# Kernel tuning notes

Measured on AMD Instinct MI355X. Metric: run time of the kernel, lower is better.

Reference implementation:

```python
import jax, jax.numpy as jnp
import numpy as np

IN_DIM, HID_DIM, OUT_DIM = 256, 1024, 256
B, T = 256, 512

def setup_inputs() -> dict:
    key = jax.random.key(0)
    ks = jax.random.split(key, 7)
    s_x = 1.0 / np.sqrt(IN_DIM)
    s_h = 1.0 / np.sqrt(HID_DIM)
    return {
        "x": jax.random.normal(ks[0], (B, T, IN_DIM), dtype=jnp.float32),
        "Wx": jax.random.uniform(ks[1], (3 * HID_DIM, IN_DIM), jnp.float32, -s_x, s_x),
        "bx": jax.random.uniform(ks[2], (3 * HID_DIM,), jnp.float32, -s_x, s_x),
        "Wh": jax.random.uniform(ks[3], (3 * HID_DIM, HID_DIM), jnp.float32, -s_h, s_h),
        "bh": jax.random.uniform(ks[4], (3 * HID_DIM,), jnp.float32, -s_h, s_h),
        "Wf": jax.random.uniform(ks[5], (OUT_DIM, HID_DIM), jnp.float32, -s_h, s_h),
        "bf": jax.random.uniform(ks[6], (OUT_DIM,), jnp.float32, -s_h, s_h),
    }

def _gru(x, Wx, bx, Wh, bh):
    # Precompute input projections for all timesteps: [B,T,3H]
    x_proj = jnp.einsum('bti,gi->btg', x, Wx) + bx
    h0 = jnp.zeros((x.shape[0], Wh.shape[1]), dtype=x.dtype)

    def step(h_prev, xp_t):
        h_t = h_prev @ Wh.T + bh  # [B,3H]
        x_r, x_z, x_n = jnp.split(xp_t, 3, axis=1)
        h_r, h_z, h_n = jnp.split(h_t, 3, axis=1)
        r = jax.nn.sigmoid(x_r + h_r)
        z = jax.nn.sigmoid(x_z + h_z)
        n = jnp.tanh(x_n + r * h_n)
        h = (1.0 - z) * h_prev + z * n  # note: nonstandard (follows source)
        return h, None

    h_final, _ = jax.lax.scan(step, h0, jnp.swapaxes(x_proj, 0, 1))
    return h_final

def reference(x, Wx, bx, Wh, bh, Wf, bf):
    h = _gru(x, Wx, bx, Wh, bh)
    return h @ Wf.T + bf  # [B, out_dim]
```

## Files before the change

### kernel.cpp

```cpp
#include <hip/hip_runtime.h>
#include <math.h>
#include <stddef.h>

#define BB 256
#define TT 512
#define IND 256
#define HH 1024
#define OUTD 256

#define INNER(ACC2)                                                            \
  _Pragma("unroll 8")                                                          \
  for (int c = 0; c < 32; ++c) {                                               \
    const float4 a  = *reinterpret_cast<const float4*>(&As[c][tb4]);           \
    const float4 w0 = *reinterpret_cast<const float4*>(&Ws[0][c][tj4]);        \
    const float4 w1 = *reinterpret_cast<const float4*>(&Ws[1][c][tj4]);        \
    const float4 w2 = *reinterpret_cast<const float4*>(&Ws[2][c][tj4]);        \
    const float av[4]  = {a.x, a.y, a.z, a.w};                                 \
    const float w0v[4] = {w0.x, w0.y, w0.z, w0.w};                             \
    const float w1v[4] = {w1.x, w1.y, w1.z, w1.w};                             \
    const float w2v[4] = {w2.x, w2.y, w2.z, w2.w};                             \
    _Pragma("unroll") for (int i = 0; i < 4; ++i) {                            \
      _Pragma("unroll") for (int l = 0; l < 4; ++l) {                          \
        acc[0][i][l] += av[i] * w0v[l];                                        \
        acc[1][i][l] += av[i] * w1v[l];                                        \
        ACC2[i][l]   += av[i] * w2v[l];                                        \
      }                                                                        \
    }                                                                          \
  }

__global__ __launch_bounds__(256) void step_gemm(
    const float* __restrict__ x, const float* __restrict__ Wx,
    const float* __restrict__ Wh, const float* __restrict__ h_prev,
    float* __restrict__ P, float* __restrict__ Pnh, int t)
{
  __shared__ float As[32][68];
  __shared__ float Ws[3][32][68];
  const int tid = threadIdx.x;
  const int b0 = blockIdx.x * 64;
  const int j0 = blockIdx.y * 64;
  const int z  = blockIdx.z;
  const int kg0 = z * 320;

  float acc[3][4][4] = {};
  float accnh[4][4]  = {};

  const int tj4 = (tid & 15) * 4;
  const int tb4 = (tid >> 4) * 4;

  const int a_row = tid >> 3;
  const int a_c4  = (tid & 7) * 4;

  for (int s = 0; s < 10; ++s) {
    const int kg = kg0 + s * 32;
    const bool isx = (kg < 256);
    __syncthreads();
    #pragma unroll
    for (int rr = 0; rr < 64; rr += 32) {
      const int b = b0 + a_row + rr;
      float4 v;
      if (isx) v = *reinterpret_cast<const float4*>(
                     &x[((size_t)b * TT + t) * IND + kg + a_c4]);
      else     v = *reinterpret_cast<const float4*>(
                     &h_prev[(size_t)b * HH + (kg - 256) + a_c4]);
      As[a_c4 + 0][a_row + rr] = v.x;
      As[a_c4 + 1][a_row + rr] = v.y;
      As[a_c4 + 2][a_row + rr] = v.z;
      As[a_c4 + 3][a_row + rr] = v.w;
    }
    #pragma unroll
    for (int p = 0; p < 6; ++p) {
      const int f   = tid + 256 * p;
      const int row = f >> 3;
      const int c4  = (f & 7) * 4;
      const int g   = row >> 6;
      const int jj  = row & 63;
      const int j   = j0 + jj;
      float4 v;
      if (isx) v = *reinterpret_cast<const float4*>(
                     &Wx[((size_t)g * HH + j) * IND + kg + c4]);
      else     v = *reinterpret_cast<const float4*>(
                     &Wh[((size_t)g * HH + j) * HH + (kg - 256) + c4]);
      Ws[g][c4 + 0][jj] = v.x;
      Ws[g][c4 + 1][jj] = v.y;
      Ws[g][c4 + 2][jj] = v.z;
      Ws[g][c4 + 3][jj] = v.w;
    }
    __syncthreads();

    const bool use_nh = (!isx) && (z == 0);
    if (use_nh) { INNER(accnh) } else { INNER(acc[2]) }
  }

  const size_t plane = (size_t)BB * HH;
  const int jout = j0 + tj4;
  #pragma unroll
  for (int g = 0; g < 3; ++g) {
    #pragma unroll
    for (int i = 0; i < 4; ++i) {
      const int b = b0 + tb4 + i;
      float4 v = {acc[g][i][0], acc[g][i][1], acc[g][i][2], acc[g][i][3]};
      *reinterpret_cast<float4*>(
        &P[((size_t)(z * 3 + g)) * plane + (size_t)b * HH + jout]) = v;
    }
  }
  if (z == 0) {
    #pragma unroll
    for (int i = 0; i < 4; ++i) {
      const int b = b0 + tb4 + i;
      float4 v = {accnh[i][0], accnh[i][1], accnh[i][2], accnh[i][3]};
      *reinterpret_cast<float4*>(&Pnh[(size_t)b * HH + jout]) = v;
    }
  }
}

__global__ __launch_bounds__(256) void gate_kernel(
    const float* __restrict__ P, const float* __restrict__ Pnh,
    const float* __restrict__ bx, const float* __restrict__ bh,
    const float* __restrict__ h_prev, float* __restrict__ h_next)
{
  const int cell = blockIdx.x * 256 + threadIdx.x;
  const int j = cell & (HH - 1);
  const size_t bj = (size_t)cell;
  const size_t plane = (size_t)BB * HH;

  float sr = bx[j] + bh[j];
  float sz = bx[HH + j] + bh[HH + j];
  #pragma unroll
  for (int k = 0; k < 4; ++k) {
    sr += P[((size_t)(k * 3 + 0)) * plane + bj];
    sz += P[((size_t)(k * 3 + 1)) * plane + bj];
  }
  float xn = P[2 * plane + bj] + bx[2 * HH + j];
  float hn = Pnh[bj] + bh[2 * HH + j];
  #pragma unroll
  for (int k = 1; k < 4; ++k) hn += P[((size_t)(k * 3 + 2)) * plane + bj];

  const float r  = 1.f / (1.f + __expf(-sr));
  const float zz = 1.f / (1.f + __expf(-sz));
  const float n  = tanhf(xn + r * hn);
  const float hp = h_prev[bj];
  h_next[bj] = (1.f - zz) * hp + zz * n;
}

__global__ __launch_bounds__(256) void final_gemm(
    const float* __restrict__ h, const float* __restrict__ Wf,
    const float* __restrict__ bf, float* __restrict__ out)
{
  __shared__ float As[32][36];
  __shared__ float Ws[32][36];
  const int tid = threadIdx.x;
  const int b0 = blockIdx.x * 32, o0 = blockIdx.y * 32;
  const int to = tid & 31, tb = tid >> 5;
  float acc[4] = {};
  for (int kc = 0; kc < HH; kc += 32) {
    __syncthreads();
    #pragma unroll
    for (int p = 0; p < 4; ++p) {
      const int f = tid + 256 * p;
      const int row = f >> 5, c = f & 31;
      As[c][row] = h[(size_t)(b0 + row) * HH + kc + c];
      Ws[c][row] = Wf[(size_t)(o0 + row) * HH + kc + c];
    }
    __syncthreads();
    #pragma unroll
    for (int c = 0; c < 32; ++c) {
      const float4 a = *reinterpret_cast<const float4*>(&As[c][tb * 4]);
      const float w = Ws[c][to];
      acc[0] += a.x * w; acc[1] += a.y * w; acc[2] += a.z * w; acc[3] += a.w * w;
    }
  }
  #pragma unroll
  for (int i = 0; i < 4; ++i)
    out[(size_t)(b0 + tb * 4 + i) * OUTD + o0 + to] = acc[i] + bf[o0 + to];
}

__global__ void zero_h(float* __restrict__ h)
{
  const int i = blockIdx.x * 256 + threadIdx.x;
  reinterpret_cast<float4*>(h)[i] = float4{0.f, 0.f, 0.f, 0.f};
}

extern "C" void kernel_launch(void* const* d_in, const int* in_sizes, int n_in,
                              void* d_out, int out_size, void* d_ws, size_t ws_size,
                              hipStream_t stream)
{
  const float* x  = (const float*)d_in[0];
  const float* Wx = (const float*)d_in[1];
  const float* bx = (const float*)d_in[2];
  const float* Wh = (const float*)d_in[3];
  const float* bh = (const float*)d_in[4];
  const float* Wf = (const float*)d_in[5];
  const float* bf = (const float*)d_in[6];
  float* out = (float*)d_out;

  float* ws = (float*)d_ws;
  const size_t plane = (size_t)BB * HH;
  float* h0  = ws;
  float* h1  = ws + plane;
  float* P   = ws + 2 * plane;
  float* Pnh = ws + 14 * plane;

  zero_h<<<256, 256, 0, stream>>>(h0);

  float* cur = h0;
  float* nxt = h1;
  for (int t = 0; t < TT; ++t) {
    step_gemm<<<dim3(4, 16, 4), 256, 0, stream>>>(x, Wx, Wh, cur, P, Pnh, t);
    gate_kernel<<<dim3(1024), 256, 0, stream>>>(P, Pnh, bx, bh, cur, nxt);
    float* tmp = cur; cur = nxt; nxt = tmp;
  }
  final_gemm<<<dim3(8, 8), 256, 0, stream>>>(cur, Wf, bf, out);
}
```

Measured before the change: 23.91 ms.

## Use split-bf16 MFMA GEMM with fused gates in a single per-step kernel

Result: slower. 30.09 ms (+25.9%).

```diff
diff --git a/kernel.cpp b/kernel.cpp
--- a/kernel.cpp
+++ b/kernel.cpp
@@ -8,138 +8,162 @@
 #define HH 1024
 #define OUTD 256
 
-#define INNER(ACC2)                                                            \
-  _Pragma("unroll 8")                                                          \
-  for (int c = 0; c < 32; ++c) {                                               \
-    const float4 a  = *reinterpret_cast<const float4*>(&As[c][tb4]);           \
-    const float4 w0 = *reinterpret_cast<const float4*>(&Ws[0][c][tj4]);        \
-    const float4 w1 = *reinterpret_cast<const float4*>(&Ws[1][c][tj4]);        \
-    const float4 w2 = *reinterpret_cast<const float4*>(&Ws[2][c][tj4]);        \
-    const float av[4]  = {a.x, a.y, a.z, a.w};                                 \
-    const float w0v[4] = {w0.x, w0.y, w0.z, w0.w};                             \
-    const float w1v[4] = {w1.x, w1.y, w1.z, w1.w};                             \
-    const float w2v[4] = {w2.x, w2.y, w2.z, w2.w};                             \
-    _Pragma("unroll") for (int i = 0; i < 4; ++i) {                            \
-      _Pragma("unroll") for (int l = 0; l < 4; ++l) {                          \
-        acc[0][i][l] += av[i] * w0v[l];                                        \
-        acc[1][i][l] += av[i] * w1v[l];                                        \
-        ACC2[i][l]   += av[i] * w2v[l];                                        \
-      }                                                                        \
-    }                                                                          \
-  }
-
-__global__ __launch_bounds__(256) void step_gemm(
-    const float* __restrict__ x, const float* __restrict__ Wx,
-    const float* __restrict__ Wh, const float* __restrict__ h_prev,
-    float* __restrict__ P, float* __restrict__ Pnh, int t)
-{
-  __shared__ float As[32][68];
-  __shared__ float Ws[3][32][68];
-  const int tid = threadIdx.x;
-  const int b0 = blockIdx.x * 64;
-  const int j0 = blockIdx.y * 64;
-  const int z  = blockIdx.z;
-  const int kg0 = z * 320;
-
-  float acc[3][4][4] = {};
-  float accnh[4][4]  = {};
-
-  const int tj4 = (tid & 15) * 4;
-  const int tb4 = (tid >> 4) * 4;
-
-  const int a_row = tid >> 3;
-  const int a_c4  = (tid & 7) * 4;
-
-  for (int s = 0; s < 10; ++s) {
-    const int kg = kg0 + s * 32;
-    const bool isx = (kg < 256);
-    __syncthreads();
-    #pragma unroll
-    for (int rr = 0; rr < 64; rr += 32) {
-      const int b = b0 + a_row + rr;
-      float4 v;
-      if (isx) v = *reinterpret_cast<const float4*>(
-                     &x[((size_t)b * TT + t) * IND + kg + a_c4]);
-      else     v = *reinterpret_cast<const float4*>(
-                     &h_prev[(size_t)b * HH + (kg - 256) + a_c4]);
-      As[a_c4 + 0][a_row + rr] = v.x;
-      As[a_c4 + 1][a_row + rr] = v.y;
-      As[a_c4 + 2][a_row + rr] = v.z;
-      As[a_c4 + 3][a_row + rr] = v.w;
-    }
-    #pragma unroll
-    for (int p = 0; p < 6; ++p) {
-      const int f   = tid + 256 * p;
-      const int row = f >> 3;
-      const int c4  = (f & 7) * 4;
-      const int g   = row >> 6;
-      const int jj  = row & 63;
-      const int j   = j0 + jj;
-      float4 v;
-      if (isx) v = *reinterpret_cast<const float4*>(
-                     &Wx[((size_t)g * HH + j) * IND + kg + c4]);
-      else     v = *reinterpret_cast<const float4*>(
-                     &Wh[((size_t)g * HH + j) * HH + (kg - 256) + c4]);
-      Ws[g][c4 + 0][jj] = v.x;
-      Ws[g][c4 + 1][jj] = v.y;
-      Ws[g][c4 + 2][jj] = v.z;
-      Ws[g][c4 + 3][jj] = v.w;
-    }
-    __syncthreads();
-
-    const bool use_nh = (!isx) && (z == 0);
-    if (use_nh) { INNER(accnh) } else { INNER(acc[2]) }
-  }
-
-  const size_t plane = (size_t)BB * HH;
-  const int jout = j0 + tj4;
+typedef __attribute__((ext_vector_type(8))) short short8;
+typedef __attribute__((ext_vector_type(4))) float f32x4;
+
+#define MFMA __builtin_amdgcn_mfma_f32_16x16x32_bf16
+
+__device__ __forceinline__ unsigned short bf16_rne(float f) {
+  unsigned u = __builtin_bit_cast(unsigned, f);
+  u += 0x7FFFu + ((u >> 16) & 1u);
+  return (unsigned short)(u >> 16);
+}
+__device__ __forceinline__ float bf16_f(unsigned short h) {
+  unsigned u = ((unsigned)h) << 16;
+  return __builtin_bit_cast(float, u);
+}
+__device__ __forceinline__ void split3(float v, unsigned short& hi,
+                                       unsigned short& mi, unsigned short& lo) {
+  hi = bf16_rne(v);
+  float r = v - bf16_f(hi);
+  mi = bf16_rne(r);
+  float r2 = r - bf16_f(mi);
+  lo = bf16_rne(r2);
+}
+
+__global__ __launch_bounds__(256) void split_w(
+    const float* __restrict__ src, int n, unsigned short* __restrict__ hi,
+    unsigned short* __restrict__ mi, unsigned short* __restrict__ lo)
+{
+  int i = blockIdx.x * 256 + threadIdx.x;
+  if (i >= n) return;
+  unsigned short a, b, c;
+  split3(src[i], a, b, c);
+  hi[i] = a; mi[i] = b; lo[i] = c;
+}
+
+__global__ __launch_bounds__(256) void init_h(
+    float* __restrict__ hf, unsigned short* __restrict__ ht)
+{
+  const int i = blockIdx.x * 256 + threadIdx.x;
+  hf[i] = 0.f;
+  ht[i] = 0; ht[i + BB * HH] = 0; ht[i + 2 * BB * HH] = 0;
+}
+
+__global__ __launch_bounds__(256, 1) void gru_step(
+    const float* __restrict__ x,
+    const unsigned short* __restrict__ Wxs,
+    const unsigned short* __restrict__ Whs,
+    const float* __restrict__ bx, const float* __restrict__ bh,
+    const float* __restrict__ hprev_f,
+    const unsigned short* __restrict__ hprev_t,
+    float* __restrict__ hnext_f,
+    unsigned short* __restrict__ hnext_t,
+    int t)
+{
+  const int id  = blockIdx.x;
+  const int xcd = id & 7;
+  const int sub = id >> 3;
+  const int jt  = xcd * 8 + (sub & 7);
+  const int bt  = sub >> 3;
+
+  const int lane = threadIdx.x & 63;
+  const int wv   = threadIdx.x >> 6;
+  const int lrow = lane & 15;
+  const int lko  = lane >> 4;
+  const int b0 = bt * 64;
+  const int j0 = jt * 16;
+  const int arow = b0 + wv * 16 + lrow;
+
+  f32x4 acc0[4] = {{0,0,0,0},{0,0,0,0},{0,0,0,0},{0,0,0,0}};
+  f32x4 acc1[4] = {{0,0,0,0},{0,0,0,0},{0,0,0,0},{0,0,0,0}};
+
+  const size_t hplane = (size_t)BB * HH;
+
+#define SIXMFMA(GI)                                                            \
+  acc0[GI] = MFMA(a_hi, b_hi, acc0[GI], 0, 0, 0);                              \
+  acc1[GI] = MFMA(a_hi, b_mi, acc1[GI], 0, 0, 0);                              \
+  acc0[GI] = MFMA(a_mi, b_hi, acc0[GI], 0, 0, 0);                              \
+  acc1[GI] = MFMA(a_hi, b_lo, acc1[GI], 0, 0, 0);                              \
+  acc0[GI] = MFMA(a_mi, b_mi, acc0[GI], 0, 0, 0);                              \
+  acc1[GI] = MFMA(a_lo, b_hi, acc1[GI], 0, 0, 0);
+
+  {
+    const float* xbase = x + ((size_t)arow * TT + t) * IND;
+    #pragma unroll 2
+    for (int kc = 0; kc < 8; ++kc) {
+      const int k = kc * 32 + lko * 8;
+      float xv[8];
+      *reinterpret_cast<float4*>(&xv[0]) =
+          *reinterpret_cast<const float4*>(&xbase[k]);
+      *reinterpret_cast<float4*>(&xv[4]) =
+          *reinterpret_cast<const float4*>(&xbase[k + 4]);
+      short8 a_hi, a_mi, a_lo;
+      #pragma unroll
+      for (int e = 0; e < 8; ++e) {
+        unsigned short h_, m_, l_;
+        split3(xv[e], h_, m_, l_);
+        a_hi[e] = (short)h_; a_mi[e] = (short)m_; a_lo[e] = (short)l_;
+      }
+      #pragma unroll
+      for (int g = 0; g < 3; ++g) {
+        const unsigned short* wp =
+            Wxs + (size_t)(g * HH + j0 + lrow) * IND + k;
+        const short8 b_hi = *reinterpret_cast<const short8*>(wp);
+        const short8 b_mi = *reinterpret_cast<const short8*>(wp + (size_t)3072 * IND);
+        const short8 b_lo = *reinterpret_cast<const short8*>(wp + (size_t)2 * 3072 * IND);
+        if (g == 0)      { SIXMFMA(0) }
+        else if (g == 1) { SIXMFMA(1) }
+        else             { SIXMFMA(2) }
+      }
+    }
+  }
+
+  {
+    const unsigned short* hb = hprev_t + (size_t)arow * HH;
+    #pragma unroll 4
+    for (int kc = 0; kc < 32; ++kc) {
+      const int k = kc * 32 + lko * 8;
+      const short8 a_hi = *reinterpret_cast<const short8*>(hb + k);
+      const short8 a_mi = *reinterpret_cast<const short8*>(hb + hplane + k);
+      const short8 a_lo = *reinterpret_cast<const short8*>(hb + 2 * hplane + k);
+      #pragma unroll
+      for (int g = 0; g < 3; ++g) {
+        const unsigned short* wp =
+            Whs + (size_t)(g * HH + j0 + lrow) * HH + k;
+        const short8 b_hi = *reinterpret_cast<const short8*>(wp);
+        const short8 b_mi = *reinterpret_cast<const short8*>(wp + (size_t)3072 * HH);
+        const short8 b_lo = *reinterpret_cast<const short8*>(wp + (size_t)2 * 3072 * HH);
+        if (g == 0)      { SIXMFMA(0) }
+        else if (g == 1) { SIXMFMA(1) }
+        else             { SIXMFMA(3) }
+      }
+    }
+  }
+
+  const int j = j0 + lrow;
+  const float bxr = bx[j],          bhr = bh[j];
+  const float bxz = bx[HH + j],     bhz = bh[HH + j];
+  const float bxn = bx[2 * HH + j], bhn = bh[2 * HH + j];
   #pragma unroll
-  for (int g = 0; g < 3; ++g) {
-    #pragma unroll
-    for (int i = 0; i < 4; ++i) {
-      const int b = b0 + tb4 + i;
-      float4 v = {acc[g][i][0], acc[g][i][1], acc[g][i][2], acc[g][i][3]};
-      *reinterpret_cast<float4*>(
-        &P[((size_t)(z * 3 + g)) * plane + (size_t)b * HH + jout]) = v;
-    }
-  }
-  if (z == 0) {
-    #pragma unroll
-    for (int i = 0; i < 4; ++i) {
-      const int b = b0 + tb4 + i;
-      float4 v = {accnh[i][0], accnh[i][1], accnh[i][2], accnh[i][3]};
-      *reinterpret_cast<float4*>(&Pnh[(size_t)b * HH + jout]) = v;
-    }
-  }
-}
-
-__global__ __launch_bounds__(256) void gate_kernel(
-    const float* __restrict__ P, const float* __restrict__ Pnh,
-    const float* __restrict__ bx, const float* __restrict__ bh,
-    const float* __restrict__ h_prev, float* __restrict__ h_next)
-{
-  const int cell = blockIdx.x * 256 + threadIdx.x;
-  const int j = cell & (HH - 1);
-  const size_t bj = (size_t)cell;
-  const size_t plane = (size_t)BB * HH;
-
-  float sr = bx[j] + bh[j];
-  float sz = bx[HH + j] + bh[HH + j];
-  #pragma unroll
-  for (int k = 0; k < 4; ++k) {
-    sr += P[((size_t)(k * 3 + 0)) * plane + bj];
-    sz += P[((size_t)(k * 3 + 1)) * plane + bj];
-  }
-  float xn = P[2 * plane + bj] + bx[2 * HH + j];
-  float hn = Pnh[bj] + bh[2 * HH + j];
-  #pragma unroll
-  for (int k = 1; k < 4; ++k) hn += P[((size_t)(k * 3 + 2)) * plane + bj];
-
-  const float r  = 1.f / (1.f + __expf(-sr));
-  const float zz = 1.f / (1.f + __expf(-sz));
-  const float n  = tanhf(xn + r * hn);
-  const float hp = h_prev[bj];
-  h_next[bj] = (1.f - zz) * hp + zz * n;
+  for (int i = 0; i < 4; ++i) {
+    const int row = b0 + wv * 16 + lko * 4 + i;
+    const float sr = acc0[0][i] + acc1[0][i] + bxr + bhr;
+    const float sz = acc0[1][i] + acc1[1][i] + bxz + bhz;
+    const float xn = acc0[2][i] + acc1[2][i] + bxn;
+    const float hn = acc0[3][i] + acc1[3][i] + bhn;
+    const float r  = 1.f / (1.f + __expf(-sr));
+    const float z  = 1.f / (1.f + __expf(-sz));
+    const float n  = tanhf(xn + r * hn);
+    const float hp = hprev_f[(size_t)row * HH + j];
+    const float hv = (1.f - z) * hp + z * n;
+    hnext_f[(size_t)row * HH + j] = hv;
+    unsigned short th, tm, tl;
+    split3(hv, th, tm, tl);
+    hnext_t[(size_t)row * HH + j] = th;
+    hnext_t[hplane + (size_t)row * HH + j] = tm;
+    hnext_t[2 * hplane + (size_t)row * HH + j] = tl;
+  }
 }
 
 __global__ __launch_bounds__(256) void final_gemm(
@@ -174,12 +198,6 @@
     out[(size_t)(b0 + tb * 4 + i) * OUTD + o0 + to] = acc[i] + bf[o0 + to];
 }
 
-__global__ void zero_h(float* __restrict__ h)
-{
-  const int i = blockIdx.x * 256 + threadIdx.x;
-  reinterpret_cast<float4*>(h)[i] = float4{0.f, 0.f, 0.f, 0.f};
-}
-
 extern "C" void kernel_launch(void* const* d_in, const int* in_sizes, int n_in,
                               void* d_out, int out_size, void* d_ws, size_t ws_size,
                               hipStream_t stream)
@@ -193,21 +211,30 @@
   const float* bf = (const float*)d_in[6];
   float* out = (float*)d_out;
 
-  float* ws = (float*)d_ws;
-  const size_t plane = (size_t)BB * HH;
-  float* h0  = ws;
-  float* h1  = ws + plane;
-  float* P   = ws + 2 * plane;
-  float* Pnh = ws + 14 * plane;
-
-  zero_h<<<256, 256, 0, stream>>>(h0);
-
-  float* cur = h0;
-  float* nxt = h1;
+  float* wsf = (float*)d_ws;
+  float* hf0 = wsf;
+  float* hf1 = wsf + (size_t)BB * HH;
+  unsigned short* u = (unsigned short*)(wsf + 2 * (size_t)BB * HH);
+  unsigned short* Whs = u;
+  unsigned short* Wxs = Whs + (size_t)3 * 3072 * HH;
+  unsigned short* ht0 = Wxs + (size_t)3 * 3072 * IND;
+  unsigned short* ht1 = ht0 + (size_t)3 * BB * HH;
+
+  const int nWh = 3 * HH * HH;
+  const int nWx = 3 * HH * IND;
+  split_w<<<dim3((nWh + 255) / 256), 256, 0, stream>>>(
+      Wh, nWh, Whs, Whs + (size_t)3072 * HH, Whs + (size_t)2 * 3072 * HH);
+  split_w<<<dim3((nWx + 255) / 256), 256, 0, stream>>>(
+      Wx, nWx, Wxs, Wxs + (size_t)3072 * IND, Wxs + (size_t)2 * 3072 * IND);
+  init_h<<<dim3(1024), 256, 0, stream>>>(hf0, ht0);
+
+  float* cf = hf0; float* nf = hf1;
+  unsigned short* ct = ht0; unsigned short* nt_ = ht1;
   for (int t = 0; t < TT; ++t) {
-    step_gemm<<<dim3(4, 16, 4), 256, 0, stream>>>(x, Wx, Wh, cur, P, Pnh, t);
-    gate_kernel<<<dim3(1024), 256, 0, stream>>>(P, Pnh, bx, bh, cur, nxt);
-    float* tmp = cur; cur = nxt; nxt = tmp;
-  }
-  final_gemm<<<dim3(8, 8), 256, 0, stream>>>(cur, Wf, bf, out);
-}
+    gru_step<<<dim3(256), 256, 0, stream>>>(x, Wxs, Whs, bx, bh,
+                                            cf, ct, nf, nt_, t);
+    float* tf = cf; cf = nf; nf = tf;
+    unsigned short* tt = ct; ct = nt_; nt_ = tt;
+  }
+  final_gemm<<<dim3(8, 8), 256, 0, stream>>>(cf, Wf, bf, out);
+}
```
